# Optimization experiments

Measured on AMD Instinct MI355X. Metric: run time of the kernel, lower is better.

## Reference

```python
import jax, jax.numpy as jnp
import numpy as np

DILATION = 1
THETA = 1.0
K = 3 + 2 * (DILATION - 1)  # 3x3 window


def setup_inputs() -> dict:
    key = jax.random.key(0)
    x = jax.random.normal(key, (8, 64, 224, 224), dtype=jnp.float32)
    return {"x": x}


def _extract_patches(x, k, d):
    # x: [b, c, h, w] -> patches: [b, c, k*k, h, w], zero-padded like F.unfold(padding=d)
    b, c, h, w = x.shape
    xp = jnp.pad(x, ((0, 0), (0, 0), (d, d), (d, d)))
    return jnp.stack(
        [xp[:, :, i * d:i * d + h, j * d:j * d + w] for i in range(k) for j in range(k)],
        axis=2,
    )


def reference(x) -> jnp.ndarray:
    b, c, h, w = x.shape
    patches = _extract_patches(x, K, DILATION)  # [b, c, kk, h, w]

    mean = patches.mean(axis=2, keepdims=True)
    # torch .std() is unbiased (ddof=1)
    std = jnp.clip(jnp.std(patches, axis=2, keepdims=True, ddof=1), 1e-3, None)
    normed = (patches - mean) / std

    contrast = (normed ** 2).mean(axis=2)
    energy = (patches ** 2).mean(axis=2)
    clamped = jnp.clip(patches, 1e-6, None)
    entropy = -(clamped * jnp.log(clamped)).mean(axis=2)
    homogeneity = 1.0 / ((1.0 + jnp.abs(patches - mean)).mean(axis=2) + 1e-6)

    feats = jnp.stack([contrast, energy, entropy, homogeneity], axis=2)  # [b, c, 4, h, w]

    log_feat = jnp.log(jnp.clip(feats, 1e-5, None))
    martingale = jnp.clip(jnp.exp(THETA * log_feat - 0.5 * THETA ** 2), 1e-4, 1e4)
    martingale = jnp.where(jnp.isfinite(martingale), martingale, jnp.ones_like(martingale))

    # per-channel feature stacks concatenated along channel dim -> [b, c*4, h, w]
    return martingale.reshape(b, c * 4, h, w)
```

## Files before the change

kernel.cpp:

```cpp
#include <hip/hip_runtime.h>
#include <math.h>

#define B 8
#define C 64
#define H 224
#define W 224
#define HW (H * W)
#define TW 32
#define TH 32

__global__ __launch_bounds__(256, 4) void medseg_kernel(const float* __restrict__ x,
                                                        float* __restrict__ out) {
    const int plane = blockIdx.z;
    const int w0 = blockIdx.x * TW;
    const int h0 = blockIdx.y * TH;
    const int tid = threadIdx.x;
    const int tx = tid & 7;
    const int ty = tid >> 3;

    const float* __restrict__ xp = x + (size_t)plane * HW;

    const int cb = w0 + 4 * tx;
    const int h  = h0 + ty;

    float win[3][12];
    const float4 Z = make_float4(0.f, 0.f, 0.f, 0.f);
    #pragma unroll
    for (int i = 0; i < 3; ++i) {
        const int r = h - 1 + i;
        const bool rin = (r >= 0) && (r < H);
        const float* rowp = xp + r * W;
        float4 a = (rin && cb > 0)     ? *(const float4*)(rowp + cb - 4) : Z;
        float4 b = rin                 ? *(const float4*)(rowp + cb)     : Z;
        float4 c = (rin && cb + 4 < W) ? *(const float4*)(rowp + cb + 4) : Z;
        win[i][0] = a.x; win[i][1]  = a.y; win[i][2]  = a.z; win[i][3]  = a.w;
        win[i][4] = b.x; win[i][5]  = b.y; win[i][6]  = b.z; win[i][7]  = b.w;
        win[i][8] = c.x; win[i][9]  = c.y; win[i][10] = c.z; win[i][11] = c.w;
    }

    float cs[6], cq[6], ce[6];
    #pragma unroll
    for (int j = 0; j < 6; ++j) {
        const float v0 = win[0][j + 3], v1 = win[1][j + 3], v2 = win[2][j + 3];
        cs[j] = v0 + v1 + v2;
        cq[j] = fmaf(v0, v0, fmaf(v1, v1, v2 * v2));
        const float c0 = fmaxf(v0, 1e-6f), c1 = fmaxf(v1, 1e-6f), c2 = fmaxf(v2, 1e-6f);
        ce[j] = fmaf(c0, __log2f(c0), fmaf(c1, __log2f(c1), c2 * __log2f(c2)));
    }

    const float EXPM  = 0.6065306597126334f;
    const float E9    = EXPM / 9.0f;
    const float NL9   = -0.6931471805599453f * EXPM / 9.0f;
    const float CONTR = 0.5391383641890075f;

    float oe[4], ot[4], oh[4];

    #pragma unroll
    for (int k = 0; k < 4; ++k) {
        const float s1 = cs[k] + cs[k + 1] + cs[k + 2];
        const float s2 = cq[k] + cq[k + 1] + cq[k + 2];
        const float se = ce[k] + ce[k + 1] + ce[k + 2];
        const float mean = s1 * (1.0f / 9.0f);

        float sad = 0.0f;
        #pragma unroll
        for (int i = 0; i < 3; ++i)
            #pragma unroll
            for (int j = 0; j < 3; ++j)
                sad += fabsf(win[i][k + j + 3] - mean);

        oe[k] = fmaxf(s2 * E9, 1e-4f);
        ot[k] = fmaxf(se * NL9, 1e-4f);
        const float denom = fmaf(sad, 1.0f / 9.0f, 1.000001f);
        oh[k] = fmaxf(EXPM * __builtin_amdgcn_rcpf(denom), 1e-4f);
    }

    float* ob = out + ((size_t)plane * 4) * HW + (size_t)h * W + cb;
    *(float4*)(ob + 0 * HW) = make_float4(CONTR, CONTR, CONTR, CONTR);
    *(float4*)(ob + 1 * HW) = make_float4(oe[0], oe[1], oe[2], oe[3]);
    *(float4*)(ob + 2 * HW) = make_float4(ot[0], ot[1], ot[2], ot[3]);
    *(float4*)(ob + 3 * HW) = make_float4(oh[0], oh[1], oh[2], oh[3]);
}

extern "C" void kernel_launch(void* const* d_in, const int* in_sizes, int n_in,
                              void* d_out, int out_size, void* d_ws, size_t ws_size,
                              hipStream_t stream) {
    const float* x = (const float*)d_in[0];
    float* out = (float*)d_out;
    dim3 grid(W / TW, H / TH, B * C);
    dim3 block(256);
    medseg_kernel<<<grid, block, 0, stream>>>(x, out);
}
```

Measured before the change: 541.1 us.

## Process four rows per thread with a rolling 3-row window and row-level log reuse

Each thread now computes four consecutive output rows instead of one and keeps a rolling three-row register window, loading only one new row per iteration. Per-row x*log(x) values are cached, so each input element's log is computed once rather than three times. Block size drops to 64 threads while the grid stays the same. This cuts redundant global loads and transcendental work, but it lowers thread-level parallelism and may hurt latency hiding in what is a memory-bound kernel.

After: 503.8 us. 1.07x faster.

```diff
diff --git a/kernel.cpp b/kernel.cpp
--- a/kernel.cpp
+++ b/kernel.cpp
@@ -8,78 +8,118 @@
 #define HW (H * W)
 #define TW 32
 #define TH 32
+#define HS 4
 
-__global__ __launch_bounds__(256, 4) void medseg_kernel(const float* __restrict__ x,
-                                                        float* __restrict__ out) {
+__global__ __launch_bounds__(64, 4) void medseg_kernel(const float* __restrict__ x,
+                                                       float* __restrict__ out) {
     const int plane = blockIdx.z;
     const int w0 = blockIdx.x * TW;
-    const int h0 = blockIdx.y * TH;
     const int tid = threadIdx.x;
     const int tx = tid & 7;
-    const int ty = tid >> 3;
+    const int g  = tid >> 3;
+    const int cb = w0 + 4 * tx;
+    const int h0 = blockIdx.y * TH + g * HS;
 
     const float* __restrict__ xp = x + (size_t)plane * HW;
+    const float4 Z = make_float4(0.f, 0.f, 0.f, 0.f);
 
-    const int cb = w0 + 4 * tx;
-    const int h  = h0 + ty;
+    const bool lb = (cb > 0);
+    const bool rb = (cb + 4 < W);
 
     float win[3][12];
-    const float4 Z = make_float4(0.f, 0.f, 0.f, 0.f);
-    #pragma unroll
-    for (int i = 0; i < 3; ++i) {
-        const int r = h - 1 + i;
+    float re[3][6];
+
+    auto loadrow = [&](int r, float w[12]) {
         const bool rin = (r >= 0) && (r < H);
         const float* rowp = xp + r * W;
-        float4 a = (rin && cb > 0)     ? *(const float4*)(rowp + cb - 4) : Z;
-        float4 b = rin                 ? *(const float4*)(rowp + cb)     : Z;
-        float4 c = (rin && cb + 4 < W) ? *(const float4*)(rowp + cb + 4) : Z;
-        win[i][0] = a.x; win[i][1]  = a.y; win[i][2]  = a.z; win[i][3]  = a.w;
-        win[i][4] = b.x; win[i][5]  = b.y; win[i][6]  = b.z; win[i][7]  = b.w;
-        win[i][8] = c.x; win[i][9]  = c.y; win[i][10] = c.z; win[i][11] = c.w;
-    }
+        float4 a = (rin && lb) ? *(const float4*)(rowp + cb - 4) : Z;
+        float4 b = rin         ? *(const float4*)(rowp + cb)     : Z;
+        float4 c = (rin && rb) ? *(const float4*)(rowp + cb + 4) : Z;
+        w[0] = a.x; w[1] = a.y; w[2]  = a.z; w[3]  = a.w;
+        w[4] = b.x; w[5] = b.y; w[6]  = b.z; w[7]  = b.w;
+        w[8] = c.x; w[9] = c.y; w[10] = c.z; w[11] = c.w;
+    };
+    auto rowstats = [&](const float w[12], float e[6]) {
+        #pragma unroll
+        for (int j = 0; j < 6; ++j) {
+            const float c0 = fmaxf(w[j + 3], 1e-6f);
+            e[j] = c0 * __log2f(c0);
+        }
+    };
 
-    float cs[6], cq[6], ce[6];
-    #pragma unroll
-    for (int j = 0; j < 6; ++j) {
-        const float v0 = win[0][j + 3], v1 = win[1][j + 3], v2 = win[2][j + 3];
-        cs[j] = v0 + v1 + v2;
-        cq[j] = fmaf(v0, v0, fmaf(v1, v1, v2 * v2));
-        const float c0 = fmaxf(v0, 1e-6f), c1 = fmaxf(v1, 1e-6f), c2 = fmaxf(v2, 1e-6f);
-        ce[j] = fmaf(c0, __log2f(c0), fmaf(c1, __log2f(c1), c2 * __log2f(c2)));
-    }
+    loadrow(h0 - 1, win[0]);
+    loadrow(h0,     win[1]);
+    loadrow(h0 + 1, win[2]);
+    rowstats(win[0], re[0]);
+    rowstats(win[1], re[1]);
+    rowstats(win[2], re[2]);
 
     const float EXPM  = 0.6065306597126334f;
     const float E9    = EXPM / 9.0f;
     const float NL9   = -0.6931471805599453f * EXPM / 9.0f;
     const float CONTR = 0.5391383641890075f;
 
-    float oe[4], ot[4], oh[4];
+    float* ob0 = out + ((size_t)plane * 4) * HW + (size_t)h0 * W + cb;
 
     #pragma unroll
-    for (int k = 0; k < 4; ++k) {
-        const float s1 = cs[k] + cs[k + 1] + cs[k + 2];
-        const float s2 = cq[k] + cq[k + 1] + cq[k + 2];
-        const float se = ce[k] + ce[k + 1] + ce[k + 2];
-        const float mean = s1 * (1.0f / 9.0f);
+    for (int it = 0; it < HS; ++it) {
+        const int s0 = it % 3, s1 = (it + 1) % 3, s2 = (it + 2) % 3;
 
-        float sad = 0.0f;
+        float4 na = Z, nb = Z, nc = Z;
+        if (it < HS - 1) {
+            const int r = h0 + it + 2;
+            const bool rin = (r < H);
+            const float* rowp = xp + r * W;
+            na = (rin && lb) ? *(const float4*)(rowp + cb - 4) : Z;
+            nb = rin         ? *(const float4*)(rowp + cb)     : Z;
+            nc = (rin && rb) ? *(const float4*)(rowp + cb + 4) : Z;
+        }
+
+        float cs[6], cq[6], ce[6];
         #pragma unroll
-        for (int i = 0; i < 3; ++i)
+        for (int j = 0; j < 6; ++j) {
+            const float v0 = win[s0][j + 3], v1 = win[s1][j + 3], v2 = win[s2][j + 3];
+            cs[j] = v0 + v1 + v2;
+            cq[j] = fmaf(v0, v0, fmaf(v1, v1, v2 * v2));
+            ce[j] = re[s0][j] + (re[s1][j] + re[s2][j]);
+        }
+
+        float oe[4], ot[4], oh[4];
+        #pragma unroll
+        for (int k = 0; k < 4; ++k) {
+            const float s1v = cs[k] + cs[k + 1] + cs[k + 2];
+            const float s2v = cq[k] + cq[k + 1] + cq[k + 2];
+            const float sev = ce[k] + ce[k + 1] + ce[k + 2];
+            const float mean = s1v * (1.0f / 9.0f);
+
+            float sad = 0.0f;
             #pragma unroll
-            for (int j = 0; j < 3; ++j)
-                sad += fabsf(win[i][k + j + 3] - mean);
+            for (int j = 0; j < 3; ++j) sad += fabsf(win[s0][k + j + 3] - mean);
+            #pragma unroll
+            for (int j = 0; j < 3; ++j) sad += fabsf(win[s1][k + j + 3] - mean);
+            #pragma unroll
+            for (int j = 0; j < 3; ++j) sad += fabsf(win[s2][k + j + 3] - mean);
 
-        oe[k] = fmaxf(s2 * E9, 1e-4f);
-        ot[k] = fmaxf(se * NL9, 1e-4f);
-        const float denom = fmaf(sad, 1.0f / 9.0f, 1.000001f);
-        oh[k] = fmaxf(EXPM * __builtin_amdgcn_rcpf(denom), 1e-4f);
+            oe[k] = fmaxf(s2v * E9, 1e-4f);
+            ot[k] = fmaxf(sev * NL9, 1e-4f);
+            const float denom = fmaf(sad, 1.0f / 9.0f, 1.000001f);
+            oh[k] = fmaxf(EXPM * __builtin_amdgcn_rcpf(denom), 1e-4f);
+        }
+
+        float* ob = ob0 + (size_t)it * W;
+        *(float4*)(ob + 0 * HW) = make_float4(CONTR, CONTR, CONTR, CONTR);
+        *(float4*)(ob + 1 * HW) = make_float4(oe[0], oe[1], oe[2], oe[3]);
+        *(float4*)(ob + 2 * HW) = make_float4(ot[0], ot[1], ot[2], ot[3]);
+        *(float4*)(ob + 3 * HW) = make_float4(oh[0], oh[1], oh[2], oh[3]);
+
+        if (it < HS - 1) {
+            float* w = win[s0];
+            w[0] = na.x; w[1] = na.y; w[2]  = na.z; w[3]  = na.w;
+            w[4] = nb.x; w[5] = nb.y; w[6]  = nb.z; w[7]  = nb.w;
+            w[8] = nc.x; w[9] = nc.y; w[10] = nc.z; w[11] = nc.w;
+            rowstats(w, re[s0]);
+        }
     }
-
-    float* ob = out + ((size_t)plane * 4) * HW + (size_t)h * W + cb;
-    *(float4*)(ob + 0 * HW) = make_float4(CONTR, CONTR, CONTR, CONTR);
-    *(float4*)(ob + 1 * HW) = make_float4(oe[0], oe[1], oe[2], oe[3]);
-    *(float4*)(ob + 2 * HW) = make_float4(ot[0], ot[1], ot[2], ot[3]);
-    *(float4*)(ob + 3 * HW) = make_float4(oh[0], oh[1], oh[2], oh[3]);
 }
 
 extern "C" void kernel_launch(void* const* d_in, const int* in_sizes, int n_in,
@@ -88,6 +128,6 @@
     const float* x = (const float*)d_in[0];
     float* out = (float*)d_out;
     dim3 grid(W / TW, H / TH, B * C);
-    dim3 block(256);
+    dim3 block(64);
     medseg_kernel<<<grid, block, 0, stream>>>(x, out);
 }
```
